# Optimization experiments

Measured on AMD Instinct MI355X. Metric: run time of the kernel, lower is better.

## Reference

```python
import jax, jax.numpy as jnp
import numpy as np

B, S, D, HEADS = 2, 2048, 1600, 25
EPS = 1e-5


def setup_inputs() -> dict:
    key = jax.random.key(0)
    ks = jax.random.split(key, 6)
    d = D
    w = lambda k, shape: (jax.random.normal(k, shape, jnp.float32) * 0.02)
    return {
        "x": jax.random.normal(ks[0], (B, S, d), jnp.float32),
        "g1": jnp.ones((d,), jnp.float32),
        "b1": jnp.zeros((d,), jnp.float32),
        "w_qkv": w(ks[1], (d, 3 * d)),
        "bias_qkv": jnp.zeros((3 * d,), jnp.float32),
        "w_proj": w(ks[2], (d, d)),
        "bias_proj": jnp.zeros((d,), jnp.float32),
        "g2": jnp.ones((d,), jnp.float32),
        "b2": jnp.zeros((d,), jnp.float32),
        "w_fc": w(ks[3], (d, 4 * d)),
        "bias_fc": jnp.zeros((4 * d,), jnp.float32),
        "w_out": w(ks[4], (4 * d, d)),
        "bias_out": jnp.zeros((d,), jnp.float32),
    }


def _layernorm(x, g, b):
    m = jnp.mean(x, axis=-1, keepdims=True)
    v = jnp.mean(jnp.square(x - m), axis=-1, keepdims=True)
    return (x - m) * jax.lax.rsqrt(v + EPS) * g + b


def reference(x, g1, b1, w_qkv, bias_qkv, w_proj, bias_proj, g2, b2, w_fc, bias_fc, w_out, bias_out):
    b, s, d = x.shape
    h = HEADS
    c = d // h  # head dim = 64

    # --- attention sub-block (pre-norm) ---
    x0 = x
    xn = _layernorm(x, g1, b1)
    qkv = xn @ w_qkv + bias_qkv  # (b, s, 3d)
    q, k, v = jnp.split(qkv, 3, axis=-1)
    q = q * (c ** -0.5)
    qh = q.reshape(b, s, h, c)
    kh = k.reshape(b, s, h, c)
    vh = v.reshape(b, s, h, c)

    # scores: (b, q, k, h) — same layout as einx.dot in the original
    scores = jnp.einsum('bqhc,bkhc->bqkh', qh, kh)
    mask = jnp.tril(jnp.ones((s, s), dtype=bool))  # causal
    scores = jnp.where(mask[None, :, :, None], scores, -jnp.inf)
    attn = jax.nn.softmax(scores, axis=2)  # softmax over k axis

    out = jnp.einsum('bqkh,bkhc->bqhc', attn, vh).reshape(b, s, d)
    x = out @ w_proj + bias_proj + x0

    # --- MLP sub-block (pre-norm) ---
    x0 = x
    xn = _layernorm(x, g2, b2)
    hdn = jax.nn.gelu(xn @ w_fc + bias_fc)  # default (tanh-approx) gelu as in jax.nn.gelu
    x = hdn @ w_out + bias_out + x0
    return x
```

## Files before the change

### kernel.cpp

```cpp
#include <hip/hip_runtime.h>
#include <math.h>

#define S_ 2048
#define D_ 1600
#define H_ 25

typedef unsigned short u16;
typedef __attribute__((ext_vector_type(8))) short short8;
typedef __attribute__((ext_vector_type(16))) float f32x16;

static __device__ __forceinline__ u16 f2h(float f) {
    union { _Float16 h; u16 u; } c;
    c.h = (_Float16)f;
    return c.u;
}

__device__ __forceinline__ float gelu_f(float x) {
    float x3 = x * x * x;
    return 0.5f * x * (1.0f + tanhf(0.7978845608028654f * (x + 0.044715f * x3)));
}

__device__ __forceinline__ int swz(int row, int col) {
    return row * 64 + ((((col >> 3) ^ row) & 7) << 3) + (col & 7);
}

__global__ __launch_bounds__(256) void wconv_kernel(
    const float* __restrict__ W, int ldW, u16* __restrict__ T, int K, int N)
{
    __shared__ __align__(16) float tile[32][33];
    const int tid = threadIdx.x;
    const int n0 = blockIdx.x * 32;
    const int k0 = blockIdx.y * 32;
    const int r = tid >> 3, cq = tid & 7;
    if (n0 < N) {
        const float4 v = *(const float4*)(W + (size_t)(k0 + r) * ldW + n0 + cq * 4);
        tile[r][cq * 4 + 0] = v.x; tile[r][cq * 4 + 1] = v.y;
        tile[r][cq * 4 + 2] = v.z; tile[r][cq * 4 + 3] = v.w;
    }
    __syncthreads();
    const int n = tid >> 3, kq = tid & 7;
    ushort4 hv = make_ushort4(0, 0, 0, 0);
    if (n0 < N) {
        hv = make_ushort4(f2h(tile[kq * 4 + 0][n]), f2h(tile[kq * 4 + 1][n]),
                          f2h(tile[kq * 4 + 2][n]), f2h(tile[kq * 4 + 3][n]));
    }
    *(ushort4*)(T + (size_t)(n0 + n) * K + k0 + kq * 4) = hv;
}

__global__ __launch_bounds__(256) void ln_f16_kernel(
    const float* __restrict__ x, const float* __restrict__ g,
    const float* __restrict__ bb, u16* __restrict__ y)
{
    const int row = blockIdx.x;
    const float* xr = x + (size_t)row * D_;
    const int tid = threadIdx.x;

    float4 a0 = ((const float4*)xr)[tid];
    float4 a1 = make_float4(0.f, 0.f, 0.f, 0.f);
    const bool has2 = tid < (D_ / 4 - 256);
    if (has2) a1 = ((const float4*)xr)[256 + tid];

    float s  = a0.x + a0.y + a0.z + a0.w + a1.x + a1.y + a1.z + a1.w;
    float s2 = a0.x*a0.x + a0.y*a0.y + a0.z*a0.z + a0.w*a0.w
             + a1.x*a1.x + a1.y*a1.y + a1.z*a1.z + a1.w*a1.w;

    #pragma unroll
    for (int m = 32; m >= 1; m >>= 1) {
        s  += __shfl_xor(s,  m);
        s2 += __shfl_xor(s2, m);
    }
    __shared__ float red[8];
    const int lane = tid & 63, wv = tid >> 6;
    if (lane == 0) { red[wv] = s; red[4 + wv] = s2; }
    __syncthreads();
    if (tid == 0) {
        red[0] = red[0] + red[1] + red[2] + red[3];
        red[4] = red[4] + red[5] + red[6] + red[7];
    }
    __syncthreads();
    const float mean = red[0] * (1.f / D_);
    const float var  = red[4] * (1.f / D_) - mean * mean;
    const float rstd = rsqrtf(var + 1e-5f);

    u16* yr = y + (size_t)row * D_;
    float4 gv = ((const float4*)g)[tid];
    float4 bv = ((const float4*)bb)[tid];
    ((ushort4*)yr)[tid] = make_ushort4(
        f2h((a0.x - mean) * rstd * gv.x + bv.x),
        f2h((a0.y - mean) * rstd * gv.y + bv.y),
        f2h((a0.z - mean) * rstd * gv.z + bv.z),
        f2h((a0.w - mean) * rstd * gv.w + bv.w));
    if (has2) {
        gv = ((const float4*)g)[256 + tid];
        bv = ((const float4*)bb)[256 + tid];
        ((ushort4*)yr)[256 + tid] = make_ushort4(
            f2h((a1.x - mean) * rstd * gv.x + bv.x),
            f2h((a1.y - mean) * rstd * gv.y + bv.y),
            f2h((a1.z - mean) * rstd * gv.z + bv.z),
            f2h((a1.w - mean) * rstd * gv.w + bv.w));
    }
}

template<int EPI, int AMODE>
__global__ __launch_bounds__(256, 4) void mgemm(
    const char* __restrict__ Ab, long lda, const u16* __restrict__ B,
    const float* __restrict__ bias, const float* __restrict__ R,
    float* __restrict__ C, u16* __restrict__ Ch,
    int ldc, int N, int K)
{
    __shared__ __align__(16) u16 sm[2][4096];
    const int tid = threadIdx.x;

    const int gx = gridDim.x;
    const int nwg = gx * (int)gridDim.y;
    const int bid0 = blockIdx.y * gx + blockIdx.x;
    const int cpx = nwg >> 3;
    const int bid = (bid0 & 7) * cpx + (bid0 >> 3);
    const int bn = (bid % gx) * 128;
    const int bm = (bid / gx) * 128;

    const int lrow  = tid & 31;
    const int lhalf = (tid >> 5) & 1;
    const int wid   = tid >> 6;
    const int wr = (wid >> 1) * 64;
    const int wc = (wid & 1) * 64;

    f32x16 acc[2][2];
    #pragma unroll
    for (int mt = 0; mt < 2; ++mt)
        #pragma unroll
        for (int nt = 0; nt < 2; ++nt)
            #pragma unroll
            for (int i = 0; i < 16; ++i) acc[mt][nt][i] = 0.f;

    for (int k0 = 0; k0 < K; k0 += 32) {
        #pragma unroll
        for (int p = 0; p < 2; ++p) {
            const int idx = p * 256 + tid;
            const int r = idx >> 2, pch = idx & 3;
            const int c = pch ^ ((r >> 1) & 3);
            const int ke = k0 + c * 8;
            const size_t ka = (AMODE == 0) ? (size_t)ke * 2
                                           : (size_t)(((ke >> 6) << 8) + ((ke & 63) << 1));
            __builtin_amdgcn_global_load_lds((const u16*)(Ab + (size_t)(bm + r) * lda + ka),
                                             &sm[0][idx * 8], 16, 0, 0);
            __builtin_amdgcn_global_load_lds(B + (size_t)(bn + r) * K + ke,
                                             &sm[1][idx * 8], 16, 0, 0);
        }
        __syncthreads();
        #pragma unroll
        for (int kc = 0; kc < 2; ++kc) {
            short8 fa[2], fb[2];
            const int ch = kc * 2 + lhalf;
            #pragma unroll
            for (int mt = 0; mt < 2; ++mt) {
                const int rr = wr + mt * 32 + lrow;
                fa[mt] = *(const short8*)&sm[0][rr * 32 + ((ch ^ ((rr >> 1) & 3)) << 3)];
            }
            #pragma unroll
            for (int nt = 0; nt < 2; ++nt) {
                const int rr = wc + nt * 32 + lrow;
                fb[nt] = *(const short8*)&sm[1][rr * 32 + ((ch ^ ((rr >> 1) & 3)) << 3)];
            }
            #pragma unroll
            for (int mt = 0; mt < 2; ++mt)
                #pragma unroll
                for (int nt = 0; nt < 2; ++nt)
                    acc[mt][nt] = __builtin_amdgcn_mfma_f32_32x32x16_f16(fa[mt], fb[nt], acc[mt][nt], 0, 0, 0);
        }
        __syncthreads();
    }

    #pragma unroll
    for (int mt = 0; mt < 2; ++mt) {
        #pragma unroll
        for (int nt = 0; nt < 2; ++nt) {
            const int col = bn + wc + nt * 32 + lrow;
            if (col < N) {
                const float bsv = bias[col];
                #pragma unroll
                for (int i = 0; i < 16; ++i) {
                    const int row = bm + wr + mt * 32 + (i & 3) + 8 * (i >> 2) + 4 * lhalf;
                    float v = acc[mt][nt][i] + bsv;
                    const size_t o = (size_t)row * ldc + col;
                    if (EPI == 0) {
                        C[o] = v;
                    } else if (EPI == 1) {
                        C[o] = v + R[o];
                    } else {
                        Ch[o] = f2h(gelu_f(v));
                    }
                }
            }
        }
    }
}

__global__ __launch_bounds__(256, 3) void attn_mfma(float* __restrict__ qkv)
{
    __shared__ __align__(16) u16 Qs[128 * 64];
    __shared__ __align__(16) u16 Ks[64 * 64];
    __shared__ __align__(16) u16 Vt[64 * 64];
    __shared__ __align__(16) u16 Ps[4][32 * 64];

    const int tid = threadIdx.x;
    const int lane = tid & 63;
    const int wid = tid >> 6;
    const int l31 = lane & 31;
    const int lh  = lane >> 5;
    const int qi = (int)gridDim.x - 1 - (int)blockIdx.x;
    const int q0 = qi * 128;
    const int bh = blockIdx.y;
    const int bb = bh / H_;
    const int h  = bh % H_;
    float* base = qkv + (size_t)bb * S_ * (3 * D_) + h * 64;

    #pragma unroll
    for (int p = 0; p < 8; ++p) {
        const int idx = p * 256 + tid;
        const int r = idx >> 4, c4 = (idx & 15) << 2;
        const float4 v = *(const float4*)(base + (size_t)(q0 + r) * (3 * D_) + c4);
        *(ushort4*)&Qs[swz(r, c4)] = make_ushort4(
            f2h(v.x * 0.125f), f2h(v.y * 0.125f), f2h(v.z * 0.125f), f2h(v.w * 0.125f));
    }
    __syncthreads();

    short8 fq[4];
    const int qrow = wid * 32 + l31;
    #pragma unroll
    for (int m = 0; m < 4; ++m)
        fq[m] = *(const short8*)&Qs[swz(qrow, m * 16 + lh * 8)];

    f32x16 o0, o1;
    #pragma unroll
    for (int i = 0; i < 16; ++i) { o0[i] = 0.f; o1[i] = 0.f; }
    float m_run = -INFINITY, l_run = 0.f;
    const int wq0 = q0 + wid * 32;
    const int myq = wq0 + l31;
    const int ntiles = q0 / 64 + 2;

    for (int t = 0; t < ntiles; ++t) {
        const int k0 = t * 64;
        __syncthreads();
        #pragma unroll
        for (int p = 0; p < 4; ++p) {
            const int idx = p * 256 + tid;
            const int r = idx >> 4, c4 = (idx & 15) << 2;
            const float* krow = base + D_ + (size_t)(k0 + r) * (3 * D_);
            const float4 kv = *(const float4*)(krow + c4);
            *(ushort4*)&Ks[swz(r, c4)] = make_ushort4(f2h(kv.x), f2h(kv.y), f2h(kv.z), f2h(kv.w));
            const float4 vv = *(const float4*)(krow + D_ + c4);
            Vt[swz(c4 + 0, r)] = f2h(vv.x);
            Vt[swz(c4 + 1, r)] = f2h(vv.y);
            Vt[swz(c4 + 2, r)] = f2h(vv.z);
            Vt[swz(c4 + 3, r)] = f2h(vv.w);
        }
        __syncthreads();

        if (k0 < wq0 + 32) {
            f32x16 s0, s1;
            #pragma unroll
            for (int i = 0; i < 16; ++i) { s0[i] = 0.f; s1[i] = 0.f; }
            #pragma unroll
            for (int m = 0; m < 4; ++m) {
                const int co = m * 16 + lh * 8;
                short8 k0f = *(const short8*)&Ks[swz(l31, co)];
                short8 k1f = *(const short8*)&Ks[swz(32 + l31, co)];
                s0 = __builtin_amdgcn_mfma_f32_32x32x16_f16(k0f, fq[m], s0, 0, 0, 0);
                s1 = __builtin_amdgcn_mfma_f32_32x32x16_f16(k1f, fq[m], s1, 0, 0, 0);
            }

            float smax = -INFINITY;
            #pragma unroll
            for (int i = 0; i < 16; ++i) {
                const int kb = (i & 3) + 8 * (i >> 2) + 4 * lh;
                float x0 = (k0 + kb > myq) ? -INFINITY : s0[i];
                float x1 = (k0 + 32 + kb > myq) ? -INFINITY : s1[i];
                s0[i] = x0; s1[i] = x1;
                smax = fmaxf(smax, fmaxf(x0, x1));
            }
            smax = fmaxf(smax, __shfl_xor(smax, 32));
            const float mn = fmaxf(m_run, smax);
            const float sc = __expf(m_run - mn);
            m_run = mn;
            float ls = 0.f;
            #pragma unroll
            for (int i = 0; i < 16; ++i) {
                const float p0 = __expf(s0[i] - mn);
                const float p1 = __expf(s1[i] - mn);
                s0[i] = p0; s1[i] = p1;
                ls += p0 + p1;
            }
            ls += __shfl_xor(ls, 32);
            l_run = l_run * sc + ls;

            #pragma unroll
            for (int j = 0; j < 8; ++j) {
                const int i = 2 * j;
                const int kb = (i & 3) + 8 * (i >> 2) + 4 * lh;
                unsigned pk0 = (unsigned)f2h(s0[i]) | ((unsigned)f2h(s0[i + 1]) << 16);
                unsigned pk1 = (unsigned)f2h(s1[i]) | ((unsigned)f2h(s1[i + 1]) << 16);
                *(unsigned*)&Ps[wid][swz(l31, kb)]      = pk0;
                *(unsigned*)&Ps[wid][swz(l31, 32 + kb)] = pk1;
            }

            float scs[16];
            #pragma unroll
            for (int i = 0; i < 16; ++i)
                scs[i] = __shfl(sc, (i & 3) + 8 * (i >> 2) + 4 * lh);
            #pragma unroll
            for (int i = 0; i < 16; ++i) { o0[i] *= scs[i]; o1[i] *= scs[i]; }

            #pragma unroll
            for (int m = 0; m < 4; ++m) {
                const int co = m * 16 + lh * 8;
                short8 fp  = *(const short8*)&Ps[wid][swz(l31, co)];
                short8 fv0 = *(const short8*)&Vt[swz(l31, co)];
                short8 fv1 = *(const short8*)&Vt[swz(32 + l31, co)];
                o0 = __builtin_amdgcn_mfma_f32_32x32x16_f16(fp, fv0, o0, 0, 0, 0);
                o1 = __builtin_amdgcn_mfma_f32_32x32x16_f16(fp, fv1, o1, 0, 0, 0);
            }
        }
    }

    const float inv = 1.f / l_run;
    #pragma unroll
    for (int i = 0; i < 16; ++i) {
        const int ri = (i & 3) + 8 * (i >> 2) + 4 * lh;
        const float sci = __shfl(inv, ri);
        u16* ph = (u16*)(base + (size_t)(q0 + wid * 32 + ri) * (3 * D_));
        ph[l31]      = f2h(o0[i] * sci);
        ph[32 + l31] = f2h(o1[i] * sci);
    }
}

extern "C" void kernel_launch(void* const* d_in, const int* in_sizes, int n_in,
                              void* d_out, int out_size, void* d_ws, size_t ws_size,
                              hipStream_t stream) {
    const float* x         = (const float*)d_in[0];
    const float* g1        = (const float*)d_in[1];
    const float* b1        = (const float*)d_in[2];
    const float* w_qkv     = (const float*)d_in[3];
    const float* bias_qkv  = (const float*)d_in[4];
    const float* w_proj    = (const float*)d_in[5];
    const float* bias_proj = (const float*)d_in[6];
    const float* g2        = (const float*)d_in[7];
    const float* b2        = (const float*)d_in[8];
    const float* w_fc      = (const float*)d_in[9];
    const float* bias_fc   = (const float*)d_in[10];
    const float* w_out     = (const float*)d_in[11];
    const float* bias_out  = (const float*)d_in[12];
    float* out = (float*)d_out;
    char* W = (char*)d_ws;

    u16*   xn  = (u16*)  (W + 0);
    float* x1  = (float*)(W + 13107200);
    float* qkv = (float*)(W + 39321600);
    u16*   hdn = (u16*)  (W + 39321600);
    u16*   wT  = (u16*)  (W + 117964800);

    dim3 blk(256);

    ln_f16_kernel<<<4096, blk, 0, stream>>>(x, g1, b1, xn);

    wconv_kernel<<<dim3(152, 50), blk, 0, stream>>>(w_qkv, 4800, wT, 1600, 4800);
    mgemm<0, 0><<<dim3(38, 32), blk, 0, stream>>>(
        (const char*)xn, 3200L, wT, bias_qkv, nullptr, qkv, nullptr, 4800, 4800, 1600);

    attn_mfma<<<dim3(16, 50), blk, 0, stream>>>(qkv);

    wconv_kernel<<<dim3(56, 50), blk, 0, stream>>>(w_proj, 1600, wT, 1600, 1600);
    mgemm<1, 1><<<dim3(13, 32), blk, 0, stream>>>(
        (const char*)qkv, 19200L, wT, bias_proj, x, x1, nullptr, 1600, 1600, 1600);

    ln_f16_kernel<<<4096, blk, 0, stream>>>(x1, g2, b2, xn);

    wconv_kernel<<<dim3(200, 50), blk, 0, stream>>>(w_fc, 6400, wT, 1600, 6400);
    mgemm<2, 0><<<dim3(50, 32), blk, 0, stream>>>(
        (const char*)xn, 3200L, wT, bias_fc, nullptr, nullptr, hdn, 6400, 6400, 1600);

    wconv_kernel<<<dim3(56, 200), blk, 0, stream>>>(w_out, 1600, wT, 6400, 1600);
    mgemm<1, 0><<<dim3(13, 32), blk, 0, stream>>>(
        (const char*)hdn, 12800L, wT, bias_out, x1, out, nullptr, 1600, 1600, 6400);
}
```

Baseline: 827.3 us.

## Emit fp16 head-major Q/K/transposed V from QKV GEMM and deepen GEMM K-tile

The QKV GEMM epilogue now writes Q (pre-scaled), K and transposed V as fp16 per-head buffers instead of one fp32 qkv matrix. The attention kernel can then load tiles straight into LDS with async global-to-LDS copies, with no fp32 reads, in-loop conversion or scattered transpose stores. Attention output goes to a separate fp16 buffer. The GEMM K-step grows from 32 to 64 with a wider XOR swizzle, which doubles shared memory per block and may lower occupancy. The head-major epilogue stores are strided 2-byte writes for Q and K, which could cost bandwidth in the GEMM.

```diff
diff --git a/kernel.cpp b/kernel.cpp
--- a/kernel.cpp
+++ b/kernel.cpp
@@ -101,14 +101,15 @@
     }
 }
 
-template<int EPI, int AMODE>
+template<int EPI>
 __global__ __launch_bounds__(256, 4) void mgemm(
-    const char* __restrict__ Ab, long lda, const u16* __restrict__ B,
+    const u16* __restrict__ A, long lda, const u16* __restrict__ B,
     const float* __restrict__ bias, const float* __restrict__ R,
     float* __restrict__ C, u16* __restrict__ Ch,
+    u16* __restrict__ Qo, u16* __restrict__ Ko, u16* __restrict__ Vo,
     int ldc, int N, int K)
 {
-    __shared__ __align__(16) u16 sm[2][4096];
+    __shared__ __align__(16) u16 sm[2][8192];
     const int tid = threadIdx.x;
 
     const int gx = gridDim.x;
@@ -133,34 +134,31 @@
             #pragma unroll
             for (int i = 0; i < 16; ++i) acc[mt][nt][i] = 0.f;
 
-    for (int k0 = 0; k0 < K; k0 += 32) {
+    for (int k0 = 0; k0 < K; k0 += 64) {
         #pragma unroll
-        for (int p = 0; p < 2; ++p) {
+        for (int p = 0; p < 4; ++p) {
             const int idx = p * 256 + tid;
-            const int r = idx >> 2, pch = idx & 3;
-            const int c = pch ^ ((r >> 1) & 3);
-            const int ke = k0 + c * 8;
-            const size_t ka = (AMODE == 0) ? (size_t)ke * 2
-                                           : (size_t)(((ke >> 6) << 8) + ((ke & 63) << 1));
-            __builtin_amdgcn_global_load_lds((const u16*)(Ab + (size_t)(bm + r) * lda + ka),
+            const int r = idx >> 3, pch = idx & 7;
+            const int ke = k0 + ((pch ^ r) & 7) * 8;
+            __builtin_amdgcn_global_load_lds(A + (size_t)(bm + r) * lda + ke,
                                              &sm[0][idx * 8], 16, 0, 0);
             __builtin_amdgcn_global_load_lds(B + (size_t)(bn + r) * K + ke,
                                              &sm[1][idx * 8], 16, 0, 0);
         }
         __syncthreads();
         #pragma unroll
-        for (int kc = 0; kc < 2; ++kc) {
+        for (int kc = 0; kc < 4; ++kc) {
             short8 fa[2], fb[2];
             const int ch = kc * 2 + lhalf;
             #pragma unroll
             for (int mt = 0; mt < 2; ++mt) {
                 const int rr = wr + mt * 32 + lrow;
-                fa[mt] = *(const short8*)&sm[0][rr * 32 + ((ch ^ ((rr >> 1) & 3)) << 3)];
+                fa[mt] = *(const short8*)&sm[0][rr * 64 + (((ch ^ rr) & 7) << 3)];
             }
             #pragma unroll
             for (int nt = 0; nt < 2; ++nt) {
                 const int rr = wc + nt * 32 + lrow;
-                fb[nt] = *(const short8*)&sm[1][rr * 32 + ((ch ^ ((rr >> 1) & 3)) << 3)];
+                fb[nt] = *(const short8*)&sm[1][rr * 64 + (((ch ^ rr) & 7) << 3)];
             }
             #pragma unroll
             for (int mt = 0; mt < 2; ++mt)
@@ -171,6 +169,8 @@
         __syncthreads();
     }
 
+    const int bb = bm >> 11;
+    const int sbase = (bm & 2047);
     #pragma unroll
     for (int mt = 0; mt < 2; ++mt) {
         #pragma unroll
@@ -178,17 +178,35 @@
             const int col = bn + wc + nt * 32 + lrow;
             if (col < N) {
                 const float bsv = bias[col];
-                #pragma unroll
-                for (int i = 0; i < 16; ++i) {
-                    const int row = bm + wr + mt * 32 + (i & 3) + 8 * (i >> 2) + 4 * lhalf;
-                    float v = acc[mt][nt][i] + bsv;
-                    const size_t o = (size_t)row * ldc + col;
-                    if (EPI == 0) {
-                        C[o] = v;
-                    } else if (EPI == 1) {
-                        C[o] = v + R[o];
-                    } else {
-                        Ch[o] = f2h(gelu_f(v));
+                if (EPI != 4) {
+                    #pragma unroll
+                    for (int i = 0; i < 16; ++i) {
+                        const int row = bm + wr + mt * 32 + (i & 3) + 8 * (i >> 2) + 4 * lhalf;
+                        float v = acc[mt][nt][i] + bsv;
+                        const size_t o = (size_t)row * ldc + col;
+                        if (EPI == 1) C[o] = v + R[o];
+                        else          Ch[o] = f2h(gelu_f(v));
+                    }
+                } else if (col < 3200) {
+                    const int cr = (col < 1600) ? col : col - 1600;
+                    const float scl = (col < 1600) ? 0.125f : 1.0f;
+                    u16* P = ((col < 1600) ? Qo : Ko)
+                             + (((size_t)(bb * H_ + (cr >> 6))) << 17) + (cr & 63);
+                    #pragma unroll
+                    for (int i = 0; i < 16; ++i) {
+                        const int s = sbase + wr + mt * 32 + (i & 3) + 8 * (i >> 2) + 4 * lhalf;
+                        P[(size_t)s << 6] = f2h((acc[mt][nt][i] + bsv) * scl);
+                    }
+                } else {
+                    const int cr = col - 3200;
+                    u16* P = Vo + (((size_t)(bb * H_ + (cr >> 6))) << 17) + ((size_t)(cr & 63) << 11);
+                    #pragma unroll
+                    for (int q = 0; q < 4; ++q) {
+                        const int s = sbase + wr + mt * 32 + 8 * q + 4 * lhalf;
+                        ushort4 hv = make_ushort4(
+                            f2h(acc[mt][nt][q * 4 + 0] + bsv), f2h(acc[mt][nt][q * 4 + 1] + bsv),
+                            f2h(acc[mt][nt][q * 4 + 2] + bsv), f2h(acc[mt][nt][q * 4 + 3] + bsv));
+                        *(ushort4*)(P + s) = hv;
                     }
                 }
             }
@@ -196,7 +214,9 @@
     }
 }
 
-__global__ __launch_bounds__(256, 3) void attn_mfma(float* __restrict__ qkv)
+__global__ __launch_bounds__(256, 3) void attn_mfma(
+    const u16* __restrict__ Q16, const u16* __restrict__ K16,
+    const u16* __restrict__ V16T, u16* __restrict__ att)
 {
     __shared__ __align__(16) u16 Qs[128 * 64];
     __shared__ __align__(16) u16 Ks[64 * 64];
@@ -211,17 +231,16 @@
     const int qi = (int)gridDim.x - 1 - (int)blockIdx.x;
     const int q0 = qi * 128;
     const int bh = blockIdx.y;
-    const int bb = bh / H_;
-    const int h  = bh % H_;
-    float* base = qkv + (size_t)bb * S_ * (3 * D_) + h * 64;
-
-    #pragma unroll
-    for (int p = 0; p < 8; ++p) {
+    const u16* qb = Q16 + ((size_t)bh << 17);
+    const u16* kb = K16 + ((size_t)bh << 17);
+    const u16* vb = V16T + ((size_t)bh << 17);
+
+    #pragma unroll
+    for (int p = 0; p < 4; ++p) {
         const int idx = p * 256 + tid;
-        const int r = idx >> 4, c4 = (idx & 15) << 2;
-        const float4 v = *(const float4*)(base + (size_t)(q0 + r) * (3 * D_) + c4);
-        *(ushort4*)&Qs[swz(r, c4)] = make_ushort4(
-            f2h(v.x * 0.125f), f2h(v.y * 0.125f), f2h(v.z * 0.125f), f2h(v.w * 0.125f));
+        const int r = idx >> 3, pch = idx & 7;
+        __builtin_amdgcn_global_load_lds(qb + (size_t)(q0 + r) * 64 + ((pch ^ r) & 7) * 8,
+                                         &Qs[idx * 8], 16, 0, 0);
     }
     __syncthreads();
 
@@ -243,17 +262,14 @@
         const int k0 = t * 64;
         __syncthreads();
         #pragma unroll
-        for (int p = 0; p < 4; ++p) {
+        for (int p = 0; p < 2; ++p) {
             const int idx = p * 256 + tid;
-            const int r = idx >> 4, c4 = (idx & 15) << 2;
-            const float* krow = base + D_ + (size_t)(k0 + r) * (3 * D_);
-            const float4 kv = *(const float4*)(krow + c4);
-            *(ushort4*)&Ks[swz(r, c4)] = make_ushort4(f2h(kv.x), f2h(kv.y), f2h(kv.z), f2h(kv.w));
-            const float4 vv = *(const float4*)(krow + D_ + c4);
-            Vt[swz(c4 + 0, r)] = f2h(vv.x);
-            Vt[swz(c4 + 1, r)] = f2h(vv.y);
-            Vt[swz(c4 + 2, r)] = f2h(vv.z);
-            Vt[swz(c4 + 3, r)] = f2h(vv.w);
+            const int r = idx >> 3, pch = idx & 7;
+            const int c8 = ((pch ^ r) & 7) * 8;
+            __builtin_amdgcn_global_load_lds(kb + (size_t)(k0 + r) * 64 + c8,
+                                             &Ks[idx * 8], 16, 0, 0);
+            __builtin_amdgcn_global_load_lds(vb + ((size_t)r << 11) + k0 + c8,
+                                             &Vt[idx * 8], 16, 0, 0);
         }
         __syncthreads();
 
@@ -273,9 +289,9 @@
             float smax = -INFINITY;
             #pragma unroll
             for (int i = 0; i < 16; ++i) {
-                const int kb = (i & 3) + 8 * (i >> 2) + 4 * lh;
-                float x0 = (k0 + kb > myq) ? -INFINITY : s0[i];
-                float x1 = (k0 + 32 + kb > myq) ? -INFINITY : s1[i];
+                const int kb2 = (i & 3) + 8 * (i >> 2) + 4 * lh;
+                float x0 = (k0 + kb2 > myq) ? -INFINITY : s0[i];
+                float x1 = (k0 + 32 + kb2 > myq) ? -INFINITY : s1[i];
                 s0[i] = x0; s1[i] = x1;
                 smax = fmaxf(smax, fmaxf(x0, x1));
             }
@@ -297,11 +313,11 @@
             #pragma unroll
             for (int j = 0; j < 8; ++j) {
                 const int i = 2 * j;
-                const int kb = (i & 3) + 8 * (i >> 2) + 4 * lh;
+                const int kb2 = (i & 3) + 8 * (i >> 2) + 4 * lh;
                 unsigned pk0 = (unsigned)f2h(s0[i]) | ((unsigned)f2h(s0[i + 1]) << 16);
                 unsigned pk1 = (unsigned)f2h(s1[i]) | ((unsigned)f2h(s1[i + 1]) << 16);
-                *(unsigned*)&Ps[wid][swz(l31, kb)]      = pk0;
-                *(unsigned*)&Ps[wid][swz(l31, 32 + kb)] = pk1;
+                *(unsigned*)&Ps[wid][swz(l31, kb2)]      = pk0;
+                *(unsigned*)&Ps[wid][swz(l31, 32 + kb2)] = pk1;
             }
 
             float scs[16];
@@ -323,12 +339,13 @@
         }
     }
 
+    const int bb = bh / H_, h = bh % H_;
     const float inv = 1.f / l_run;
     #pragma unroll
     for (int i = 0; i < 16; ++i) {
         const int ri = (i & 3) + 8 * (i >> 2) + 4 * lh;
         const float sci = __shfl(inv, ri);
-        u16* ph = (u16*)(base + (size_t)(q0 + wid * 32 + ri) * (3 * D_));
+        u16* ph = att + (size_t)(bb * S_ + q0 + wid * 32 + ri) * D_ + h * 64;
         ph[l31]      = f2h(o0[i] * sci);
         ph[32 + l31] = f2h(o1[i] * sci);
     }
@@ -353,33 +370,40 @@
     float* out = (float*)d_out;
     char* W = (char*)d_ws;
 
-    u16*   xn  = (u16*)  (W + 0);
-    float* x1  = (float*)(W + 13107200);
-    float* qkv = (float*)(W + 39321600);
-    u16*   hdn = (u16*)  (W + 39321600);
-    u16*   wT  = (u16*)  (W + 117964800);
+    u16*   xn    = (u16*)  (W + 0);
+    float* x1    = (float*)(W + 13107200);
+    u16*   Q16   = (u16*)  (W + 39321600);
+    u16*   K16   = (u16*)  (W + 52428800);
+    u16*   V16T  = (u16*)  (W + 65536000);
+    u16*   att16 = (u16*)  (W + 78643200);
+    u16*   hdn   = (u16*)  (W + 39321600);
+    u16*   wT    = (u16*)  (W + 91750400);
 
     dim3 blk(256);
 
     ln_f16_kernel<<<4096, blk, 0, stream>>>(x, g1, b1, xn);
 
     wconv_kernel<<<dim3(152, 50), blk, 0, stream>>>(w_qkv, 4800, wT, 1600, 4800);
-    mgemm<0, 0><<<dim3(38, 32), blk, 0, stream>>>(
-        (const char*)xn, 3200L, wT, bias_qkv, nullptr, qkv, nullptr, 4800, 4800, 1600);
-
-    attn_mfma<<<dim3(16, 50), blk, 0, stream>>>(qkv);
-
-    wconv_kernel<<<dim3(56, 50), blk, 0, stream>>>(w_proj, 1600, wT, 1600, 1600);
-    mgemm<1, 1><<<dim3(13, 32), blk, 0, stream>>>(
-        (const char*)qkv, 19200L, wT, bias_proj, x, x1, nullptr, 1600, 1600, 1600);
+    mgemm<4><<<dim3(38, 32), blk, 0, stream>>>(
+        xn, 1600L, wT, bias_qkv, nullptr, nullptr, nullptr,
+        Q16, K16, V16T, 0, 4800, 1600);
+
+    attn_mfma<<<dim3(16, 50), blk, 0, stream>>>(Q16, K16, V16T, att16);
+
+    wconv_kernel<<<dim3(52, 50), blk, 0, stream>>>(w_proj, 1600, wT, 1600, 1600);
+    mgemm<1><<<dim3(13, 32), blk, 0, stream>>>(
+        att16, 1600L, wT, bias_proj, x, x1, nullptr,
+        nullptr, nullptr, nullptr, 1600, 1600, 1600);
 
     ln_f16_kernel<<<4096, blk, 0, stream>>>(x1, g2, b2, xn);
 
     wconv_kernel<<<dim3(200, 50), blk, 0, stream>>>(w_fc, 6400, wT, 1600, 6400);
-    mgemm<2, 0><<<dim3(50, 32), blk, 0, stream>>>(
-        (const char*)xn, 3200L, wT, bias_fc, nullptr, nullptr, hdn, 6400, 6400, 1600);
-
-    wconv_kernel<<<dim3(56, 200), blk, 0, stream>>>(w_out, 1600, wT, 6400, 1600);
-    mgemm<1, 0><<<dim3(13, 32), blk, 0, stream>>>(
-        (const char*)hdn, 12800L, wT, bias_out, x1, out, nullptr, 1600, 1600, 6400);
-}
+    mgemm<2><<<dim3(50, 32), blk, 0, stream>>>(
+        xn, 1600L, wT, bias_fc, nullptr, nullptr, hdn,
+        nullptr, nullptr, nullptr, 6400, 6400, 1600);
+
+    wconv_kernel<<<dim3(52, 200), blk, 0, stream>>>(w_out, 1600, wT, 6400, 1600);
+    mgemm<1><<<dim3(13, 32), blk, 0, stream>>>(
+        hdn, 6400L, wT, bias_out, x1, out, nullptr,
+        nullptr, nullptr, nullptr, 1600, 1600, 6400);
+}
```

New measurement: 708.6 us. -14.3%, faster.
